# Kernel optimization log

Hardware: AMD Instinct MI355X
Metric: run time of the kernel (lower is better)

The kernel has to match this reference:

```python
import jax, jax.numpy as jnp
import numpy as np


def setup_inputs() -> dict:
    key = jax.random.key(0)
    k1, k2, k3 = jax.random.split(key, 3)
    B, S, D = 32, 1024, 256
    input_real = jax.random.normal(k1, (B, S, D), dtype=jnp.float32)
    input_imag = jax.random.normal(k2, (B, S, D), dtype=jnp.float32)
    # per-token mixture weights (e.g. softmax over sequence in CFN)
    weights = jax.random.uniform(k3, (B, S), dtype=jnp.float32)
    return {"input_real": input_real, "input_imag": input_imag, "weights": weights}


def reference(input_real, input_imag, weights):
    # Original layer: out[b,a,c] = sum_s w[b,s] * (v[b,s,a] * conj(v)[b,s,c]) with v = r + i*j
    # output_real[a,c] = r[a]r[c] + i[a]i[c];  output_imag[a,c] = i[a]r[c] - r[a]i[c]
    # Weighted sum over s == V^T diag(w) V, expressed as einsum (no (B,S,D,D) intermediate).
    wr = input_real * weights[:, :, None]  # (B,S,D)
    wi = input_imag * weights[:, :, None]
    output_r = jnp.einsum('bsa,bsc->bac', wr, input_real) + jnp.einsum('bsa,bsc->bac', wi, input_imag)
    output_i = jnp.einsum('bsa,bsc->bac', wi, input_real) - jnp.einsum('bsa,bsc->bac', wr, input_imag)
    return (output_r, output_i)
```

## Files before the change

### kernel.cpp

```cpp
#include <hip/hip_runtime.h>

typedef __attribute__((ext_vector_type(8))) short s8v;
typedef __attribute__((ext_vector_type(16))) float f32x16;

#define BB 32
#define SS 1024
#define DD 256
#define KB 64
#define LSTR 72
#define PSZ (64 * LSTR)


__device__ __forceinline__ unsigned short bf16rn(float v) {
    unsigned b = __float_as_uint(v);
    return (unsigned short)((b + 0x7FFFu + ((b >> 16) & 1u)) >> 16);
}

extern "C" __global__ void __launch_bounds__(256, 2)
cmix3_kernel(const float* __restrict__ real, const float* __restrict__ imag,
             const float* __restrict__ wts, float* __restrict__ out) {
    __shared__ unsigned short lds[6 * PSZ];

    const int bx   = blockIdx.x;
    const int xcd  = bx & 7;
    const int slot = bx >> 3;
    const int b    = xcd * 4 + (slot >> 4);
    const int t    = slot & 15;
    const int a0   = (t >> 2) * 64;
    const int c0   = (t & 3) * 64;

    const int tid = threadIdx.x;
    const int wid = tid >> 6;
    const int l   = tid & 63;

    const int  fgrp = (l >> 2) & 15;
    const int  sgrp = l & 3;
    const bool isA  = (wid < 2);
    const float* srcArr = ((wid & 1) ? imag : real)
                        + (size_t)b * SS * DD + (isA ? a0 : c0) + fgrp * 4;
    const float* wb = wts + (size_t)b * SS;

    const int m0  = (wid >> 1) * 32;
    const int n0  = (wid & 1) * 32;
    const int fr  = l & 31;
    const int hi8 = (l >> 5) * 8;

    const int pA = wid * 2 * PSZ;
    const int pC = (4 + (wid & 1)) * PSZ;

    f32x16 accr = {}, acci = {}, accx = {};

    for (int ch = 0; ch < 16; ++ch) {
        const int s0 = ch * KB;
        __syncthreads();
        const int sb = s0 + sgrp * 16;

        if (isA) {
            #pragma unroll
            for (int hb = 0; hb < 2; ++hb) {
                const int sh = sb + hb * 8;
                const float4 w1 = *(const float4*)(wb + sh);
                const float4 w2 = *(const float4*)(wb + sh + 4);
                const float wv[8] = {w1.x,w1.y,w1.z,w1.w,w2.x,w2.y,w2.z,w2.w};
                unsigned hw[4][4], lw[4][4];
                #pragma unroll
                for (int si = 0; si < 8; ++si) {
                    const float4 x = *(const float4*)(srcArr + (size_t)(sh + si) * DD);
                    const float ww = wv[si];
                    const float y[4] = {x.x*ww, x.y*ww, x.z*ww, x.w*ww};
                    #pragma unroll
                    for (int e = 0; e < 4; ++e) {
                        unsigned yb   = __float_as_uint(y[e]);
                        unsigned hb32 = yb & 0xFFFF0000u;
                        float    lo   = y[e] - __uint_as_float(hb32);
                        unsigned hs   = hb32 >> 16;
                        unsigned ls   = __float_as_uint(lo) >> 16;
                        if (si & 1) { hw[e][si>>1] |= hs << 16; lw[e][si>>1] |= ls << 16; }
                        else        { hw[e][si>>1]  = hs;       lw[e][si>>1]  = ls; }
                    }
                }
                #pragma unroll
                for (int e = 0; e < 4; ++e) {
                    const int off = (fgrp*4 + e) * LSTR + sgrp*16 + hb*8;
                    uint4 vh = {hw[e][0], hw[e][1], hw[e][2], hw[e][3]};
                    uint4 vl = {lw[e][0], lw[e][1], lw[e][2], lw[e][3]};
                    *(uint4*)&lds[pA + off]       = vh;
                    *(uint4*)&lds[pA + PSZ + off] = vl;
                }
            }
        } else {
            #pragma unroll
            for (int hb = 0; hb < 2; ++hb) {
                const int sh = sb + hb * 8;
                unsigned cw[4][4];
                #pragma unroll
                for (int si = 0; si < 8; ++si) {
                    const float4 x = *(const float4*)(srcArr + (size_t)(sh + si) * DD);
                    const float y[4] = {x.x, x.y, x.z, x.w};
                    #pragma unroll
                    for (int e = 0; e < 4; ++e) {
                        unsigned cs = bf16rn(y[e]);
                        if (si & 1) cw[e][si>>1] |= cs << 16; else cw[e][si>>1] = cs;
                    }
                }
                #pragma unroll
                for (int e = 0; e < 4; ++e) {
                    const int off = (fgrp*4 + e) * LSTR + sgrp*16 + hb*8;
                    uint4 v = {cw[e][0], cw[e][1], cw[e][2], cw[e][3]};
                    *(uint4*)&lds[pC + off] = v;
                }
            }
        }
        __syncthreads();

        #pragma unroll
        for (int kk = 0; kk < 4; ++kk) {
            const int ko = kk * 16 + hi8;
            const int ra = (m0 + fr) * LSTR + ko;
            const int rc = (n0 + fr) * LSTR + ko;
            s8v A1 = *(const s8v*)&lds[0*PSZ + ra];
            s8v A2 = *(const s8v*)&lds[1*PSZ + ra];
            s8v A3 = *(const s8v*)&lds[2*PSZ + ra];
            s8v A4 = *(const s8v*)&lds[3*PSZ + ra];
            s8v C1 = *(const s8v*)&lds[4*PSZ + rc];
            s8v C2 = *(const s8v*)&lds[5*PSZ + rc];
            accr = __builtin_amdgcn_mfma_f32_32x32x16_bf16(A1, C1, accr, 0, 0, 0);
            accr = __builtin_amdgcn_mfma_f32_32x32x16_bf16(A2, C1, accr, 0, 0, 0);
            accr = __builtin_amdgcn_mfma_f32_32x32x16_bf16(A3, C2, accr, 0, 0, 0);
            accr = __builtin_amdgcn_mfma_f32_32x32x16_bf16(A4, C2, accr, 0, 0, 0);
            acci = __builtin_amdgcn_mfma_f32_32x32x16_bf16(A3, C1, acci, 0, 0, 0);
            acci = __builtin_amdgcn_mfma_f32_32x32x16_bf16(A4, C1, acci, 0, 0, 0);
            accx = __builtin_amdgcn_mfma_f32_32x32x16_bf16(A1, C2, accx, 0, 0, 0);
            accx = __builtin_amdgcn_mfma_f32_32x32x16_bf16(A2, C2, accx, 0, 0, 0);
        }
    }

    float* outR = out + (size_t)b * DD * DD;
    float* outI = out + (size_t)BB * DD * DD + (size_t)b * DD * DD;
    const int col = c0 + n0 + (l & 31);
    #pragma unroll
    for (int g = 0; g < 4; ++g) {
        #pragma unroll
        for (int q = 0; q < 4; ++q) {
            const int reg = g * 4 + q;
            const int row = a0 + m0 + q + 8 * g + 4 * (l >> 5);
            outR[(size_t)row * DD + col] = accr[reg];
            outI[(size_t)row * DD + col] = acci[reg] - accx[reg];
        }
    }
}

extern "C" void kernel_launch(void* const* d_in, const int* in_sizes, int n_in,
                              void* d_out, int out_size, void* d_ws, size_t ws_size,
                              hipStream_t stream) {
    const float* real = (const float*)d_in[0];
    const float* imag = (const float*)d_in[1];
    const float* wts  = (const float*)d_in[2];
    float* out = (float*)d_out;
    dim3 grid(512);
    dim3 block(256);
    cmix3_kernel<<<grid, block, 0, stream>>>(real, imag, wts, out);
}
```

Measured before the change: 159.9 us.

## Double-buffer LDS and prefetch next chunk into registers during MFMA

Halves the sequence chunk to 32 and allocates two LDS buffers. The next chunk's global loads are issued into registers before the current chunk's MFMAs, then converted and stored to the alternate buffer afterwards, leaving one barrier per iteration. This is meant to hide global-load latency behind matrix compute instead of serialising load, convert and compute. In exchange it holds 8 float4 prefetch registers per thread, runs twice as many smaller iterations, and uses a similar total LDS footprint.

```diff
diff --git a/kernel.cpp b/kernel.cpp
--- a/kernel.cpp
+++ b/kernel.cpp
@@ -6,9 +6,11 @@
 #define BB 32
 #define SS 1024
 #define DD 256
-#define KB 64
-#define LSTR 72
+#define KB 32
+#define NCH (SS / KB)
+#define LSTR 40
 #define PSZ (64 * LSTR)
+#define BUFS (6 * PSZ)
 
 
 __device__ __forceinline__ unsigned short bf16rn(float v) {
@@ -17,9 +19,9 @@
 }
 
 extern "C" __global__ void __launch_bounds__(256, 2)
-cmix3_kernel(const float* __restrict__ real, const float* __restrict__ imag,
+cmix4_kernel(const float* __restrict__ real, const float* __restrict__ imag,
              const float* __restrict__ wts, float* __restrict__ out) {
-    __shared__ unsigned short lds[6 * PSZ];
+    __shared__ unsigned short lds[2 * BUFS];
 
     const int bx   = blockIdx.x;
     const int xcd  = bx & 7;
@@ -33,97 +35,100 @@
     const int wid = tid >> 6;
     const int l   = tid & 63;
 
-    const int  fgrp = (l >> 2) & 15;
+    const int  fgrp = l >> 2;
     const int  sgrp = l & 3;
     const bool isA  = (wid < 2);
-    const float* srcArr = ((wid & 1) ? imag : real)
-                        + (size_t)b * SS * DD + (isA ? a0 : c0) + fgrp * 4;
+    const float* srcA = ((wid & 1) ? imag : real)
+                      + (size_t)b * SS * DD + (isA ? a0 : c0) + fgrp * 4;
     const float* wb = wts + (size_t)b * SS;
+    const int pA   = wid * 2 * PSZ;
+    const int pC   = (4 + (wid & 1)) * PSZ;
+    const int woff = fgrp * 4 * LSTR + sgrp * 8;
 
     const int m0  = (wid >> 1) * 32;
     const int n0  = (wid & 1) * 32;
     const int fr  = l & 31;
     const int hi8 = (l >> 5) * 8;
 
-    const int pA = wid * 2 * PSZ;
-    const int pC = (4 + (wid & 1)) * PSZ;
+    f32x16 accr = {}, acci = {}, accx = {};
+    float4 xr[8];
 
-    f32x16 accr = {}, acci = {}, accx = {};
+    auto stage_load = [&](int sch) {
+        const int sh = sch + sgrp * 8;
+        #pragma unroll
+        for (int si = 0; si < 8; ++si)
+            xr[si] = *(const float4*)(srcA + (size_t)(sh + si) * DD);
+    };
 
-    for (int ch = 0; ch < 16; ++ch) {
-        const int s0 = ch * KB;
-        __syncthreads();
-        const int sb = s0 + sgrp * 16;
-
+    auto stage_store = [&](unsigned short* buf, int sch) {
+        const int sh = sch + sgrp * 8;
         if (isA) {
+            const float4 w1 = *(const float4*)(wb + sh);
+            const float4 w2 = *(const float4*)(wb + sh + 4);
+            const float wv[8] = {w1.x,w1.y,w1.z,w1.w,w2.x,w2.y,w2.z,w2.w};
+            unsigned hw[4][4], lw[4][4];
             #pragma unroll
-            for (int hb = 0; hb < 2; ++hb) {
-                const int sh = sb + hb * 8;
-                const float4 w1 = *(const float4*)(wb + sh);
-                const float4 w2 = *(const float4*)(wb + sh + 4);
-                const float wv[8] = {w1.x,w1.y,w1.z,w1.w,w2.x,w2.y,w2.z,w2.w};
-                unsigned hw[4][4], lw[4][4];
-                #pragma unroll
-                for (int si = 0; si < 8; ++si) {
-                    const float4 x = *(const float4*)(srcArr + (size_t)(sh + si) * DD);
-                    const float ww = wv[si];
-                    const float y[4] = {x.x*ww, x.y*ww, x.z*ww, x.w*ww};
-                    #pragma unroll
-                    for (int e = 0; e < 4; ++e) {
-                        unsigned yb   = __float_as_uint(y[e]);
-                        unsigned hb32 = yb & 0xFFFF0000u;
-                        float    lo   = y[e] - __uint_as_float(hb32);
-                        unsigned hs   = hb32 >> 16;
-                        unsigned ls   = __float_as_uint(lo) >> 16;
-                        if (si & 1) { hw[e][si>>1] |= hs << 16; lw[e][si>>1] |= ls << 16; }
-                        else        { hw[e][si>>1]  = hs;       lw[e][si>>1]  = ls; }
-                    }
-                }
+            for (int si = 0; si < 8; ++si) {
+                const float y[4] = {xr[si].x*wv[si], xr[si].y*wv[si],
+                                    xr[si].z*wv[si], xr[si].w*wv[si]};
                 #pragma unroll
                 for (int e = 0; e < 4; ++e) {
-                    const int off = (fgrp*4 + e) * LSTR + sgrp*16 + hb*8;
-                    uint4 vh = {hw[e][0], hw[e][1], hw[e][2], hw[e][3]};
-                    uint4 vl = {lw[e][0], lw[e][1], lw[e][2], lw[e][3]};
-                    *(uint4*)&lds[pA + off]       = vh;
-                    *(uint4*)&lds[pA + PSZ + off] = vl;
+                    unsigned yb   = __float_as_uint(y[e]);
+                    unsigned hb32 = yb & 0xFFFF0000u;
+                    float    lo   = y[e] - __uint_as_float(hb32);
+                    unsigned hs   = hb32 >> 16;
+                    unsigned ls   = __float_as_uint(lo) >> 16;
+                    if (si & 1) { hw[e][si>>1] |= hs << 16; lw[e][si>>1] |= ls << 16; }
+                    else        { hw[e][si>>1]  = hs;       lw[e][si>>1]  = ls; }
                 }
             }
+            #pragma unroll
+            for (int e = 0; e < 4; ++e) {
+                uint4 vh = {hw[e][0], hw[e][1], hw[e][2], hw[e][3]};
+                uint4 vl = {lw[e][0], lw[e][1], lw[e][2], lw[e][3]};
+                *(uint4*)&buf[pA + woff + e * LSTR]       = vh;
+                *(uint4*)&buf[pA + PSZ + woff + e * LSTR] = vl;
+            }
         } else {
+            unsigned cw[4][4];
             #pragma unroll
-            for (int hb = 0; hb < 2; ++hb) {
-                const int sh = sb + hb * 8;
-                unsigned cw[4][4];
-                #pragma unroll
-                for (int si = 0; si < 8; ++si) {
-                    const float4 x = *(const float4*)(srcArr + (size_t)(sh + si) * DD);
-                    const float y[4] = {x.x, x.y, x.z, x.w};
-                    #pragma unroll
-                    for (int e = 0; e < 4; ++e) {
-                        unsigned cs = bf16rn(y[e]);
-                        if (si & 1) cw[e][si>>1] |= cs << 16; else cw[e][si>>1] = cs;
-                    }
-                }
+            for (int si = 0; si < 8; ++si) {
+                const float y[4] = {xr[si].x, xr[si].y, xr[si].z, xr[si].w};
                 #pragma unroll
                 for (int e = 0; e < 4; ++e) {
-                    const int off = (fgrp*4 + e) * LSTR + sgrp*16 + hb*8;
-                    uint4 v = {cw[e][0], cw[e][1], cw[e][2], cw[e][3]};
-                    *(uint4*)&lds[pC + off] = v;
+                    unsigned cs = bf16rn(y[e]);
+                    if (si & 1) cw[e][si>>1] |= cs << 16; else cw[e][si>>1] = cs;
                 }
             }
+            #pragma unroll
+            for (int e = 0; e < 4; ++e) {
+                uint4 v = {cw[e][0], cw[e][1], cw[e][2], cw[e][3]};
+                *(uint4*)&buf[pC + woff + e * LSTR] = v;
+            }
         }
-        __syncthreads();
+    };
+
+    stage_load(0);
+    stage_store(lds, 0);
+    __syncthreads();
+
+    for (int ch = 0; ch < NCH; ++ch) {
+        unsigned short* bc = lds + (ch & 1) * BUFS;
+        unsigned short* bs = lds + ((ch & 1) ^ 1) * BUFS;
+        const bool more = (ch + 1 < NCH);
+        if (more) stage_load((ch + 1) * KB);
 
         #pragma unroll
-        for (int kk = 0; kk < 4; ++kk) {
+        for (int kk = 0; kk < 2; ++kk) {
             const int ko = kk * 16 + hi8;
             const int ra = (m0 + fr) * LSTR + ko;
             const int rc = (n0 + fr) * LSTR + ko;
-            s8v A1 = *(const s8v*)&lds[0*PSZ + ra];
-            s8v A2 = *(const s8v*)&lds[1*PSZ + ra];
-            s8v A3 = *(const s8v*)&lds[2*PSZ + ra];
-            s8v A4 = *(const s8v*)&lds[3*PSZ + ra];
-            s8v C1 = *(const s8v*)&lds[4*PSZ + rc];
-            s8v C2 = *(const s8v*)&lds[5*PSZ + rc];
+            s8v A1 = *(const s8v*)&bc[0*PSZ + ra];
+            s8v A2 = *(const s8v*)&bc[1*PSZ + ra];
+            s8v A3 = *(const s8v*)&bc[2*PSZ + ra];
+            s8v A4 = *(const s8v*)&bc[3*PSZ + ra];
+            s8v C1 = *(const s8v*)&bc[4*PSZ + rc];
+            s8v C2 = *(const s8v*)&bc[5*PSZ + rc];
             accr = __builtin_amdgcn_mfma_f32_32x32x16_bf16(A1, C1, accr, 0, 0, 0);
             accr = __builtin_amdgcn_mfma_f32_32x32x16_bf16(A2, C1, accr, 0, 0, 0);
             accr = __builtin_amdgcn_mfma_f32_32x32x16_bf16(A3, C2, accr, 0, 0, 0);
@@ -133,6 +138,9 @@
             accx = __builtin_amdgcn_mfma_f32_32x32x16_bf16(A1, C2, accx, 0, 0, 0);
             accx = __builtin_amdgcn_mfma_f32_32x32x16_bf16(A2, C2, accx, 0, 0, 0);
         }
+
+        if (more) stage_store(bs, (ch + 1) * KB);
+        __syncthreads();
     }
 
     float* outR = out + (size_t)b * DD * DD;
@@ -159,5 +167,5 @@
     float* out = (float*)d_out;
     dim3 grid(512);
     dim3 block(256);
-    cmix3_kernel<<<grid, block, 0, stream>>>(real, imag, wts, out);
+    cmix4_kernel<<<grid, block, 0, stream>>>(real, imag, wts, out);
 }
```

Result: faster. 155.8 us (-2.6%).
